# Kernel tuning notes

Hardware: AMD Instinct MI355X
Metric: run time of the kernel (lower is better)

## Reference

```python
import jax, jax.numpy as jnp
import numpy as np

T, N, DH, E = 4, 50000, 64, 800000
BN_EPS = 1e-5


def setup_inputs() -> dict:
    key = jax.random.key(0)
    ks = jax.random.split(key, 8)
    node_data = jax.random.normal(ks[0], (T, N, DH), dtype=jnp.float32)
    edge_weight = jax.random.uniform(ks[1], (E,), dtype=jnp.float32)
    W1 = jax.random.normal(ks[2], (DH, 3 * DH), dtype=jnp.float32) * 0.05
    b1 = jax.random.normal(ks[3], (DH,), dtype=jnp.float32) * 0.05
    gamma = jnp.ones((3 * DH,), dtype=jnp.float32)
    beta = jnp.zeros((3 * DH,), dtype=jnp.float32)
    src = jax.random.randint(ks[4], (E,), 0, N)
    dst = jax.random.randint(ks[5], (E,), 0, N)
    return {"node_data": node_data, "edge_weight": edge_weight, "W1": W1,
            "b1": b1, "gamma": gamma, "beta": beta, "src": src, "dst": dst}


def reference(node_data, edge_weight, W1, b1, gamma, beta, src, dst):
    # --- sparse weighted neighbor aggregation (torch.bmm with sparse ew) ---
    # msg[t, e, :] = w_e * x[t, src_e, :]
    msg = node_data[:, src, :] * edge_weight[None, :, None]          # [T, E, dh]
    agg = jnp.zeros((T, N, DH), jnp.float32).at[:, dst, :].add(msg)  # [T, N, dh]
    # Z = torch.sparse.sum(ew, dim=2); Z[Z==0]=1 (degree normalization)
    Z = jnp.zeros((N,), jnp.float32).at[dst].add(edge_weight)
    Z = jnp.where(Z == 0, 1.0, Z)
    avg_neighbor = agg / Z[None, :, None]
    # prev_state: zeros at t=0, shifted node_data otherwise
    prev = jnp.concatenate([jnp.zeros((1, N, DH), jnp.float32), node_data[:-1]], axis=0)
    inp = jnp.concatenate([node_data, prev, avg_neighbor], axis=2).reshape(T * N, 3 * DH)
    # --- ReluFCN with batchnorm (training-mode batch stats, biased var) ---
    mu = jnp.mean(inp, axis=0)
    var = jnp.mean(jnp.square(inp - mu), axis=0)
    xhat = (inp - mu) * jax.lax.rsqrt(var + BN_EPS) * gamma + beta
    out = jax.nn.relu(xhat @ W1.T + b1)
    return out.reshape(T, N, DH)
```

## Files before the change

kernel.cpp:

```cpp
#include <hip/hip_runtime.h>

#define TT 4
#define NN 50000
#define DH 64
#define EE 800000
#define BN_EPS 1e-5f
#define NB 196
#define G1 64
#define G2 256

typedef __attribute__((ext_vector_type(8))) short short8;
typedef __attribute__((ext_vector_type(4))) float floatx4;

#define WS_DEG      0
#define WS_FLAGS    200704
#define WS_ROWSTART 201728
#define WS_PX       401920
#define WS_PX2      467456
#define WS_PA       532992
#define WS_PA2      598528
#define WS_W1EFF    664064
#define WS_B1EFF    688640
#define WS_PACKED   1048576
#define WS_XB       8388608
#define WS_AVGB     34078720
#define WS_RANK     34078720

__device__ __forceinline__ unsigned short f2b(float f) {
    unsigned int u = __float_as_uint(f);
    unsigned int r = (u + 0x7FFFu + ((u >> 16) & 1u)) >> 16;
    return (unsigned short)r;
}
__device__ __forceinline__ float b2f(unsigned short u) {
    return __uint_as_float((unsigned int)u << 16);
}

__global__ __launch_bounds__(256) void k_prep_stats(
    const float* __restrict__ x, unsigned short* __restrict__ xb,
    float* __restrict__ PX, float* __restrict__ PX2,
    int* __restrict__ deg, int* __restrict__ flags) {
    int t = blockIdx.y;
    int tid = threadIdx.x;
    int pb = t * G1 + blockIdx.x;
    int gid = pb * 256 + tid;
    if (gid < NN) deg[gid] = 0;
    else if (gid < NN + NB) flags[gid - NN] = 0;

    int g = blockIdx.x * 256 + tid;
    const floatx4* xt = (const floatx4*)(x + (size_t)t * NN * 64);
    unsigned short* xbt = xb + (size_t)t * NN * 64;
    float s[4] = {0.f, 0.f, 0.f, 0.f}, s2[4] = {0.f, 0.f, 0.f, 0.f};
    for (int v = g; v < NN * 16; v += G1 * 256) {
        floatx4 d = __builtin_nontemporal_load(&xt[v]);
        ushort4 o;
        o.x = f2b(d.x); o.y = f2b(d.y); o.z = f2b(d.z); o.w = f2b(d.w);
        *(ushort4*)(xbt + (size_t)v * 4) = o;
        s[0] += d.x; s2[0] += d.x * d.x;
        s[1] += d.y; s2[1] += d.y * d.y;
        s[2] += d.z; s2[2] += d.z * d.z;
        s[3] += d.w; s2[3] += d.w * d.w;
    }
    __shared__ float ls[256 * 4], ls2[256 * 4];
#pragma unroll
    for (int j = 0; j < 4; ++j) { ls[tid * 4 + j] = s[j]; ls2[tid * 4 + j] = s2[j]; }
    __syncthreads();
    if (tid < 64) {
        int g16 = tid >> 2, comp = tid & 3;
        float rs = 0.f, rs2 = 0.f;
#pragma unroll
        for (int k = 0; k < 16; ++k) {
            int j = g16 + 16 * k;
            rs += ls[j * 4 + comp]; rs2 += ls2[j * 4 + comp];
        }
        int slot = (t * G1 + blockIdx.x) * 64 + tid;
        PX[slot] = rs; PX2[slot] = rs2;
    }
}

__global__ void k_rank(const int* __restrict__ dst, int* __restrict__ deg,
                       int* __restrict__ rank) {
    int e = blockIdx.x * 256 + threadIdx.x;
    if (e < EE) rank[e] = atomicAdd(&deg[dst[e]], 1);
}

__global__ __launch_bounds__(256) void k_scan_lb(
    const int* __restrict__ deg, int* __restrict__ flags,
    int* __restrict__ row_start) {
    int b = blockIdx.x, tid = threadIdx.x;
    int i = b * 256 + tid;
    int v = (i < NN) ? deg[i] : 0;
    __shared__ int ls[256];
    ls[tid] = v;
    __syncthreads();
    for (int off = 1; off < 256; off <<= 1) {
        int t = (tid >= off) ? ls[tid - off] : 0;
        __syncthreads();
        ls[tid] += t;
        __syncthreads();
    }
    int incl = ls[tid];
    if (tid == 0) atomicExch(&flags[b], ls[255] + 1);
    __shared__ int pre_s;
    if (tid == 0) pre_s = 0;
    __syncthreads();
    if (tid < b) {
        int f;
        do { f = atomicAdd(&flags[tid], 0); } while (f == 0);
        atomicAdd(&pre_s, f - 1);
    }
    __syncthreads();
    int excl = pre_s + incl - v;
    if (i < NN) row_start[i] = excl;
    if (i == NN - 1) row_start[NN] = excl + v;
}

__global__ void k_fill2(const int* __restrict__ src, const int* __restrict__ dst,
                        const float* __restrict__ ew, const int* __restrict__ rank,
                        const int* __restrict__ row_start, int2* __restrict__ packed) {
    int e = blockIdx.x * 256 + threadIdx.x;
    if (e < EE) {
        int p = row_start[dst[e]] + rank[e];
        packed[p] = make_int2(src[e], __float_as_int(ew[e]));
    }
}

__global__ __launch_bounds__(256) void k_agg(
    const unsigned short* __restrict__ xb, const int2* __restrict__ packed,
    const int* __restrict__ row_start, unsigned short* __restrict__ avgb) {
    int wv = __builtin_amdgcn_readfirstlane(threadIdx.x >> 6);
    int n = blockIdx.x * 4 + wv;
    int l = threadIdx.x & 63;
    int t = l >> 4;
    int cg = (l & 15) * 4;
    const unsigned short* xt = xb + (size_t)t * NN * 64 + cg;
    int rs = row_start[n], re = row_start[n + 1];
    float a0 = 0.f, a1 = 0.f, a2 = 0.f, a3 = 0.f, wsum = 0.f;
    int e = rs;
    for (; e + 8 <= re; e += 8) {
        int2 p[8];
        ushort4 v[8];
#pragma unroll
        for (int j = 0; j < 8; ++j) p[j] = packed[e + j];
#pragma unroll
        for (int j = 0; j < 8; ++j) v[j] = *(const ushort4*)(xt + (size_t)p[j].x * 64);
#pragma unroll
        for (int j = 0; j < 8; ++j) {
            float w = __int_as_float(p[j].y);
            wsum += w;
            a0 = fmaf(w, b2f(v[j].x), a0); a1 = fmaf(w, b2f(v[j].y), a1);
            a2 = fmaf(w, b2f(v[j].z), a2); a3 = fmaf(w, b2f(v[j].w), a3);
        }
    }
    for (; e < re; ++e) {
        int2 p0 = packed[e];
        float w0 = __int_as_float(p0.y);
        ushort4 v0 = *(const ushort4*)(xt + (size_t)p0.x * 64);
        wsum += w0;
        a0 = fmaf(w0, b2f(v0.x), a0); a1 = fmaf(w0, b2f(v0.y), a1);
        a2 = fmaf(w0, b2f(v0.z), a2); a3 = fmaf(w0, b2f(v0.w), a3);
    }
    float rz = (wsum == 0.f) ? 1.f : (1.f / wsum);
    ushort4 o;
    o.x = f2b(a0 * rz); o.y = f2b(a1 * rz); o.z = f2b(a2 * rz); o.w = f2b(a3 * rz);
    *(ushort4*)(avgb + (size_t)t * NN * 64 + (size_t)n * 64 + cg) = o;
}

__global__ __launch_bounds__(256) void k_stats_avg(
    const unsigned short* __restrict__ avgb, float* __restrict__ PA,
    float* __restrict__ PA2) {
    int tid = threadIdx.x;
    int g = blockIdx.x * 256 + tid;
    const short8* av = (const short8*)avgb;
    float s[8], s2[8];
#pragma unroll
    for (int j = 0; j < 8; ++j) { s[j] = 0.f; s2[j] = 0.f; }
    for (int v = g; v < TT * NN * 8; v += G2 * 256) {
        short8 d = av[v];
#pragma unroll
        for (int j = 0; j < 8; ++j) {
            float f = b2f((unsigned short)d[j]);
            s[j] += f; s2[j] += f * f;
        }
    }
    __shared__ float ls[256 * 8], ls2[256 * 8];
#pragma unroll
    for (int j = 0; j < 8; ++j) { ls[tid * 8 + j] = s[j]; ls2[tid * 8 + j] = s2[j]; }
    __syncthreads();
    if (tid < 64) {
        int g8 = tid >> 3, comp = tid & 7;
        float rs = 0.f, rs2 = 0.f;
#pragma unroll
        for (int k = 0; k < 32; ++k) {
            int j = g8 + 8 * k;
            rs += ls[j * 8 + comp]; rs2 += ls2[j * 8 + comp];
        }
        PA[blockIdx.x * 64 + tid] = rs;
        PA2[blockIdx.x * 64 + tid] = rs2;
    }
}

__global__ void k_fold(const float* __restrict__ W1, const float* __restrict__ b1,
                       const float* __restrict__ gamma, const float* __restrict__ beta,
                       const float* __restrict__ PX, const float* __restrict__ PX2,
                       const float* __restrict__ PA, const float* __restrict__ PA2,
                       unsigned short* __restrict__ W1eff, float* __restrict__ b1eff) {
    __shared__ float gS[192], hS[192];
    int c = threadIdx.x;
    const float inv = 1.0f / (float)(TT * NN);
    if (c < 192) {
        float s = 0.f, s2 = 0.f;
        if (c < 64) {
            for (int i = 0; i < TT * G1; ++i) { s += PX[i * 64 + c]; s2 += PX2[i * 64 + c]; }
        } else if (c < 128) {
            int cc = c - 64;
            for (int i = 0; i < (TT - 1) * G1; ++i) { s += PX[i * 64 + cc]; s2 += PX2[i * 64 + cc]; }
        } else {
            int cc = c - 128;
            for (int i = 0; i < G2; ++i) { s += PA[i * 64 + cc]; s2 += PA2[i * 64 + cc]; }
        }
        float mu = s * inv, ex2 = s2 * inv;
        float var = ex2 - mu * mu;
        float g = gamma[c] / sqrtf(var + BN_EPS);
        gS[c] = g;
        hS[c] = beta[c] - mu * g;
    }
    __syncthreads();
    for (int i = threadIdx.x; i < 64 * 192; i += blockDim.x) {
        int cc = i % 192;
        W1eff[i] = f2b(W1[i] * gS[cc]);
    }
    if (threadIdx.x < 64) {
        int o = threadIdx.x;
        float acc = b1[o];
        for (int cc = 0; cc < 192; ++cc) acc += hS[cc] * W1[o * 192 + cc];
        b1eff[o] = acc;
    }
}

__global__ __launch_bounds__(256) void k_main(
    const unsigned short* __restrict__ xb, const unsigned short* __restrict__ avgb,
    const unsigned short* __restrict__ Wb, const float* __restrict__ bias,
    float* __restrict__ out) {
    int wave = threadIdx.x >> 6;
    int lane = threadIdx.x & 63;
    int r0 = blockIdx.x * 64 + wave * 16;
    int m = lane & 15;
    int q = lane >> 4;

    const unsigned short* xrow = xb   + (size_t)(r0 + m) * 64 + q * 8;
    const unsigned short* prow = xb   + (size_t)(r0 - NN + m) * 64 + q * 8;
    const unsigned short* arow = avgb + (size_t)(r0 + m) * 64 + q * 8;
    bool has_prev = (r0 >= NN);

    floatx4 acc[4];
#pragma unroll
    for (int ct = 0; ct < 4; ++ct) acc[ct] = (floatx4){0.f, 0.f, 0.f, 0.f};

    const short8 zf = (short8){0, 0, 0, 0, 0, 0, 0, 0};

#pragma unroll
    for (int kc = 0; kc < 6; ++kc) {
        short8 a;
        if (kc < 2) {
            a = *(const short8*)(xrow + kc * 32);
        } else if (kc < 4) {
            a = has_prev ? *(const short8*)(prow + (kc - 2) * 32) : zf;
        } else {
            a = *(const short8*)(arow + (kc - 4) * 32);
        }
#pragma unroll
        for (int ct = 0; ct < 4; ++ct) {
            short8 b = *(const short8*)(Wb + (size_t)(ct * 16 + m) * 192 + kc * 32 + q * 8);
            acc[ct] = __builtin_amdgcn_mfma_f32_16x16x32_bf16(a, b, acc[ct], 0, 0, 0);
        }
    }

#pragma unroll
    for (int ct = 0; ct < 4; ++ct) {
        float bv = bias[ct * 16 + m];
#pragma unroll
        for (int i = 0; i < 4; ++i) {
            int row = q * 4 + i;
            __builtin_nontemporal_store(fmaxf(acc[ct][i] + bv, 0.f),
                                        &out[(size_t)(r0 + row) * 64 + ct * 16 + m]);
        }
    }
}

extern "C" void kernel_launch(void* const* d_in, const int* in_sizes, int n_in,
                              void* d_out, int out_size, void* d_ws, size_t ws_size,
                              hipStream_t stream) {
    const float* x     = (const float*)d_in[0];
    const float* ew    = (const float*)d_in[1];
    const float* W1    = (const float*)d_in[2];
    const float* b1    = (const float*)d_in[3];
    const float* gamma = (const float*)d_in[4];
    const float* beta  = (const float*)d_in[5];
    const int*   src   = (const int*)d_in[6];
    const int*   dst   = (const int*)d_in[7];
    float* out = (float*)d_out;
    char*  ws  = (char*)d_ws;

    int*   deg      = (int*)(ws + WS_DEG);
    int*   flags    = (int*)(ws + WS_FLAGS);
    int*   row_start= (int*)(ws + WS_ROWSTART);
    float* PX       = (float*)(ws + WS_PX);
    float* PX2      = (float*)(ws + WS_PX2);
    float* PA       = (float*)(ws + WS_PA);
    float* PA2      = (float*)(ws + WS_PA2);
    unsigned short* W1eff = (unsigned short*)(ws + WS_W1EFF);
    float* b1eff    = (float*)(ws + WS_B1EFF);
    int2*  packed   = (int2*)(ws + WS_PACKED);
    unsigned short* xb   = (unsigned short*)(ws + WS_XB);
    unsigned short* avgb = (unsigned short*)(ws + WS_AVGB);
    int*   rank     = (int*)(ws + WS_RANK);

    k_prep_stats<<<dim3(G1, TT), 256, 0, stream>>>(x, xb, PX, PX2, deg, flags);

    k_rank<<<(EE + 255) / 256, 256, 0, stream>>>(dst, deg, rank);

    k_scan_lb<<<NB, 256, 0, stream>>>(deg, flags, row_start);

    k_fill2<<<(EE + 255) / 256, 256, 0, stream>>>(src, dst, ew, rank, row_start, packed);

    k_agg<<<NN / 4, 256, 0, stream>>>(xb, packed, row_start, avgb);

    k_stats_avg<<<G2, 256, 0, stream>>>(avgb, PA, PA2);

    k_fold<<<1, 192, 0, stream>>>(W1, b1, gamma, beta, PX, PX2, PA, PA2, W1eff, b1eff);

    k_main<<<(TT * NN) / 64, 256, 0, stream>>>(xb, avgb, W1eff, b1eff, out);
}
```

Baseline: 338.3 us.

## Interleave timesteps per node in bf16 buffers so gathers fetch all T rows at once

The bf16 copy of node features and the averaged-neighbor buffer move from [T][N][64] to node-major [N][T][64], so each node's four timesteps sit in one contiguous 512-byte row. The aggregation kernel then gathers a whole row per edge with 16-byte loads, and has each half-wave take alternate edges before combining them with a cross-lane shuffle. This removes the four scattered 128-byte gathers per edge of the old layout. The matmul kernel's addressing is updated for the new layout, including the previous-timestep offset. The tail loop now issues a dummy load from row 0 for padded lanes, and the stats kernel over avgb still works because it only sums per-channel values.

```diff
diff --git a/kernel.cpp b/kernel.cpp
--- a/kernel.cpp
+++ b/kernel.cpp
@@ -48,13 +48,12 @@
 
     int g = blockIdx.x * 256 + tid;
     const floatx4* xt = (const floatx4*)(x + (size_t)t * NN * 64);
-    unsigned short* xbt = xb + (size_t)t * NN * 64;
     float s[4] = {0.f, 0.f, 0.f, 0.f}, s2[4] = {0.f, 0.f, 0.f, 0.f};
     for (int v = g; v < NN * 16; v += G1 * 256) {
         floatx4 d = __builtin_nontemporal_load(&xt[v]);
         ushort4 o;
         o.x = f2b(d.x); o.y = f2b(d.y); o.z = f2b(d.z); o.w = f2b(d.w);
-        *(ushort4*)(xbt + (size_t)v * 4) = o;
+        *(ushort4*)(xb + (size_t)(v >> 4) * 256 + t * 64 + (v & 15) * 4) = o;
         s[0] += d.x; s2[0] += d.x * d.x;
         s[1] += d.y; s2[1] += d.y * d.y;
         s[2] += d.z; s2[2] += d.z * d.z;
@@ -127,42 +126,72 @@
 __global__ __launch_bounds__(256) void k_agg(
     const unsigned short* __restrict__ xb, const int2* __restrict__ packed,
     const int* __restrict__ row_start, unsigned short* __restrict__ avgb) {
-    int wv = __builtin_amdgcn_readfirstlane(threadIdx.x >> 6);
+    int wv = threadIdx.x >> 6;
     int n = blockIdx.x * 4 + wv;
     int l = threadIdx.x & 63;
-    int t = l >> 4;
-    int cg = (l & 15) * 4;
-    const unsigned short* xt = xb + (size_t)t * NN * 64 + cg;
+    int half = l >> 5;
+    int j = l & 31;
+    const unsigned short* xt = xb + (size_t)j * 8;
     int rs = row_start[n], re = row_start[n + 1];
-    float a0 = 0.f, a1 = 0.f, a2 = 0.f, a3 = 0.f, wsum = 0.f;
-    int e = rs;
-    for (; e + 8 <= re; e += 8) {
-        int2 p[8];
-        ushort4 v[8];
-#pragma unroll
-        for (int j = 0; j < 8; ++j) p[j] = packed[e + j];
-#pragma unroll
-        for (int j = 0; j < 8; ++j) v[j] = *(const ushort4*)(xt + (size_t)p[j].x * 64);
-#pragma unroll
-        for (int j = 0; j < 8; ++j) {
-            float w = __int_as_float(p[j].y);
+    float acc[8];
+#pragma unroll
+    for (int k = 0; k < 8; ++k) acc[k] = 0.f;
+    float wsum = 0.f;
+
+    int base = rs;
+    for (; base + 16 <= re; base += 16) {
+        int2 p[8]; short8 v[8];
+#pragma unroll
+        for (int i = 0; i < 8; ++i) p[i] = packed[base + 2 * i + half];
+#pragma unroll
+        for (int i = 0; i < 8; ++i) v[i] = *(const short8*)(xt + (size_t)p[i].x * 256);
+#pragma unroll
+        for (int i = 0; i < 8; ++i) {
+            float w = __int_as_float(p[i].y);
             wsum += w;
-            a0 = fmaf(w, b2f(v[j].x), a0); a1 = fmaf(w, b2f(v[j].y), a1);
-            a2 = fmaf(w, b2f(v[j].z), a2); a3 = fmaf(w, b2f(v[j].w), a3);
-        }
-    }
-    for (; e < re; ++e) {
-        int2 p0 = packed[e];
-        float w0 = __int_as_float(p0.y);
-        ushort4 v0 = *(const ushort4*)(xt + (size_t)p0.x * 64);
-        wsum += w0;
-        a0 = fmaf(w0, b2f(v0.x), a0); a1 = fmaf(w0, b2f(v0.y), a1);
-        a2 = fmaf(w0, b2f(v0.z), a2); a3 = fmaf(w0, b2f(v0.w), a3);
-    }
+#pragma unroll
+            for (int k = 0; k < 8; ++k)
+                acc[k] = fmaf(w, b2f((unsigned short)v[i][k]), acc[k]);
+        }
+    }
+    if (base + 8 <= re) {
+        int2 p[4]; short8 v[4];
+#pragma unroll
+        for (int i = 0; i < 4; ++i) p[i] = packed[base + 2 * i + half];
+#pragma unroll
+        for (int i = 0; i < 4; ++i) v[i] = *(const short8*)(xt + (size_t)p[i].x * 256);
+#pragma unroll
+        for (int i = 0; i < 4; ++i) {
+            float w = __int_as_float(p[i].y);
+            wsum += w;
+#pragma unroll
+            for (int k = 0; k < 8; ++k)
+                acc[k] = fmaf(w, b2f((unsigned short)v[i][k]), acc[k]);
+        }
+        base += 8;
+    }
+    for (; base < re; base += 2) {
+        int ee = base + half;
+        int2 p = (ee < re) ? packed[ee] : make_int2(0, 0);
+        short8 v = *(const short8*)(xt + (size_t)p.x * 256);
+        float w = __int_as_float(p.y);
+        wsum += w;
+#pragma unroll
+        for (int k = 0; k < 8; ++k)
+            acc[k] = fmaf(w, b2f((unsigned short)v[k]), acc[k]);
+    }
+
+#pragma unroll
+    for (int k = 0; k < 8; ++k) acc[k] += __shfl_xor(acc[k], 32);
+    wsum += __shfl_xor(wsum, 32);
+
     float rz = (wsum == 0.f) ? 1.f : (1.f / wsum);
-    ushort4 o;
-    o.x = f2b(a0 * rz); o.y = f2b(a1 * rz); o.z = f2b(a2 * rz); o.w = f2b(a3 * rz);
-    *(ushort4*)(avgb + (size_t)t * NN * 64 + (size_t)n * 64 + cg) = o;
+    if (half == 0) {
+        short8 o;
+#pragma unroll
+        for (int k = 0; k < 8; ++k) o[k] = (short)f2b(acc[k] * rz);
+        *(short8*)(avgb + (size_t)n * 256 + (size_t)j * 8) = o;
+    }
 }
 
 __global__ __launch_bounds__(256) void k_stats_avg(
@@ -244,13 +273,15 @@
     int wave = threadIdx.x >> 6;
     int lane = threadIdx.x & 63;
     int r0 = blockIdx.x * 64 + wave * 16;
+    int t = r0 / NN;
+    int n0 = r0 - t * NN;
     int m = lane & 15;
     int q = lane >> 4;
 
-    const unsigned short* xrow = xb   + (size_t)(r0 + m) * 64 + q * 8;
-    const unsigned short* prow = xb   + (size_t)(r0 - NN + m) * 64 + q * 8;
-    const unsigned short* arow = avgb + (size_t)(r0 + m) * 64 + q * 8;
-    bool has_prev = (r0 >= NN);
+    size_t nb = (size_t)(n0 + m) * 256 + (size_t)t * 64 + q * 8;
+    const unsigned short* xrow = xb + nb;
+    const unsigned short* arow = avgb + nb;
+    bool has_prev = (t >= 1);
 
     floatx4 acc[4];
 #pragma unroll
@@ -264,7 +295,7 @@
         if (kc < 2) {
             a = *(const short8*)(xrow + kc * 32);
         } else if (kc < 4) {
-            a = has_prev ? *(const short8*)(prow + (kc - 2) * 32) : zf;
+            a = has_prev ? *(const short8*)(xrow - 64 + (kc - 2) * 32) : zf;
         } else {
             a = *(const short8*)(arow + (kc - 4) * 32);
         }
```

After: 342.9 us. Within noise of the previous version (+1.4%).

## Interleave timesteps per node in bf16 buffers and switch kernels to grid-stride loops

Applied to the files above, without the earlier changes.

The bf16 copies of node features and neighbour averages move from a [T][N][64] layout to a node-major [N][T][64] layout. Each edge gather in the aggregation kernel then reads one contiguous 512-byte row covering all timesteps, instead of four separate 128-byte rows. The rank, fill, aggregation and matmul kernels become persistent grid-stride loops over a fixed number of blocks, and the aggregation inner loop masks its tail instead of using a separate remainder loop. The weight-folding kernel is spread over several blocks, each of which recomputes the batchnorm statistics.

```diff
diff --git a/kernel.cpp b/kernel.cpp
--- a/kernel.cpp
+++ b/kernel.cpp
@@ -8,6 +8,11 @@
 #define NB 196
 #define G1 64
 #define G2 256
+#define EB 2048
+#define AGG_B 2048
+#define AGG_W (AGG_B*4)
+#define MAIN_B 2048
+#define FOLD_B 8
 
 typedef __attribute__((ext_vector_type(8))) short short8;
 typedef __attribute__((ext_vector_type(4))) float floatx4;
@@ -48,13 +53,12 @@
 
     int g = blockIdx.x * 256 + tid;
     const floatx4* xt = (const floatx4*)(x + (size_t)t * NN * 64);
-    unsigned short* xbt = xb + (size_t)t * NN * 64;
     float s[4] = {0.f, 0.f, 0.f, 0.f}, s2[4] = {0.f, 0.f, 0.f, 0.f};
     for (int v = g; v < NN * 16; v += G1 * 256) {
         floatx4 d = __builtin_nontemporal_load(&xt[v]);
         ushort4 o;
         o.x = f2b(d.x); o.y = f2b(d.y); o.z = f2b(d.z); o.w = f2b(d.w);
-        *(ushort4*)(xbt + (size_t)v * 4) = o;
+        *(ushort4*)(xb + (size_t)(v >> 4) * 256 + t * 64 + (v & 15) * 4) = o;
         s[0] += d.x; s2[0] += d.x * d.x;
         s[1] += d.y; s2[1] += d.y * d.y;
         s[2] += d.z; s2[2] += d.z * d.z;
@@ -77,10 +81,11 @@
     }
 }
 
-__global__ void k_rank(const int* __restrict__ dst, int* __restrict__ deg,
-                       int* __restrict__ rank) {
-    int e = blockIdx.x * 256 + threadIdx.x;
-    if (e < EE) rank[e] = atomicAdd(&deg[dst[e]], 1);
+__global__ __launch_bounds__(256) void k_rank(const int* __restrict__ dst,
+                                              int* __restrict__ deg,
+                                              int* __restrict__ rank) {
+    for (int e = blockIdx.x * 256 + threadIdx.x; e < EE; e += EB * 256)
+        rank[e] = atomicAdd(&deg[dst[e]], 1);
 }
 
 __global__ __launch_bounds__(256) void k_scan_lb(
@@ -114,11 +119,11 @@
     if (i == NN - 1) row_start[NN] = excl + v;
 }
 
-__global__ void k_fill2(const int* __restrict__ src, const int* __restrict__ dst,
-                        const float* __restrict__ ew, const int* __restrict__ rank,
-                        const int* __restrict__ row_start, int2* __restrict__ packed) {
-    int e = blockIdx.x * 256 + threadIdx.x;
-    if (e < EE) {
+__global__ __launch_bounds__(256) void k_fill2(
+    const int* __restrict__ src, const int* __restrict__ dst,
+    const float* __restrict__ ew, const int* __restrict__ rank,
+    const int* __restrict__ row_start, int2* __restrict__ packed) {
+    for (int e = blockIdx.x * 256 + threadIdx.x; e < EE; e += EB * 256) {
         int p = row_start[dst[e]] + rank[e];
         packed[p] = make_int2(src[e], __float_as_int(ew[e]));
     }
@@ -128,41 +133,39 @@
     const unsigned short* __restrict__ xb, const int2* __restrict__ packed,
     const int* __restrict__ row_start, unsigned short* __restrict__ avgb) {
     int wv = __builtin_amdgcn_readfirstlane(threadIdx.x >> 6);
-    int n = blockIdx.x * 4 + wv;
     int l = threadIdx.x & 63;
-    int t = l >> 4;
-    int cg = (l & 15) * 4;
-    const unsigned short* xt = xb + (size_t)t * NN * 64 + cg;
-    int rs = row_start[n], re = row_start[n + 1];
-    float a0 = 0.f, a1 = 0.f, a2 = 0.f, a3 = 0.f, wsum = 0.f;
-    int e = rs;
-    for (; e + 8 <= re; e += 8) {
-        int2 p[8];
-        ushort4 v[8];
-#pragma unroll
-        for (int j = 0; j < 8; ++j) p[j] = packed[e + j];
-#pragma unroll
-        for (int j = 0; j < 8; ++j) v[j] = *(const ushort4*)(xt + (size_t)p[j].x * 64);
-#pragma unroll
-        for (int j = 0; j < 8; ++j) {
-            float w = __int_as_float(p[j].y);
-            wsum += w;
-            a0 = fmaf(w, b2f(v[j].x), a0); a1 = fmaf(w, b2f(v[j].y), a1);
-            a2 = fmaf(w, b2f(v[j].z), a2); a3 = fmaf(w, b2f(v[j].w), a3);
-        }
-    }
-    for (; e < re; ++e) {
-        int2 p0 = packed[e];
-        float w0 = __int_as_float(p0.y);
-        ushort4 v0 = *(const ushort4*)(xt + (size_t)p0.x * 64);
-        wsum += w0;
-        a0 = fmaf(w0, b2f(v0.x), a0); a1 = fmaf(w0, b2f(v0.y), a1);
-        a2 = fmaf(w0, b2f(v0.z), a2); a3 = fmaf(w0, b2f(v0.w), a3);
-    }
-    float rz = (wsum == 0.f) ? 1.f : (1.f / wsum);
-    ushort4 o;
-    o.x = f2b(a0 * rz); o.y = f2b(a1 * rz); o.z = f2b(a2 * rz); o.w = f2b(a3 * rz);
-    *(ushort4*)(avgb + (size_t)t * NN * 64 + (size_t)n * 64 + cg) = o;
+    int wgid = blockIdx.x * 4 + wv;
+    const ushort4* xl = (const ushort4*)xb + l;
+    for (int n = wgid; n < NN; n += AGG_W) {
+        int rs = row_start[n], re = row_start[n + 1];
+        float a0 = 0.f, a1 = 0.f, a2 = 0.f, a3 = 0.f, wsum = 0.f;
+        for (int e = rs; e < re; e += 8) {
+            int rem = re - e;
+            int2 p[8];
+#pragma unroll
+            for (int j = 0; j < 8; ++j) p[j] = packed[e + j];
+            ushort4 v[8];
+#pragma unroll
+            for (int j = 0; j < 8; ++j) {
+                int sidx = (j < rem) ? p[j].x : 0;
+                v[j] = xl[(size_t)sidx * 64];
+            }
+#pragma unroll
+            for (int j = 0; j < 8; ++j) {
+                float w = (j < rem) ? __int_as_float(p[j].y) : 0.f;
+                wsum += w;
+                a0 = fmaf(w, b2f(v[j].x), a0);
+                a1 = fmaf(w, b2f(v[j].y), a1);
+                a2 = fmaf(w, b2f(v[j].z), a2);
+                a3 = fmaf(w, b2f(v[j].w), a3);
+            }
+        }
+        float rz = (wsum == 0.f) ? 1.f : (1.f / wsum);
+        ushort4 o;
+        o.x = f2b(a0 * rz); o.y = f2b(a1 * rz);
+        o.z = f2b(a2 * rz); o.w = f2b(a3 * rz);
+        *((ushort4*)avgb + (size_t)n * 64 + l) = o;
+    }
 }
 
 __global__ __launch_bounds__(256) void k_stats_avg(
@@ -225,12 +228,10 @@
         hS[c] = beta[c] - mu * g;
     }
     __syncthreads();
-    for (int i = threadIdx.x; i < 64 * 192; i += blockDim.x) {
-        int cc = i % 192;
-        W1eff[i] = f2b(W1[i] * gS[cc]);
-    }
-    if (threadIdx.x < 64) {
-        int o = threadIdx.x;
+    for (int i = blockIdx.x * 192 + c; i < 64 * 192; i += FOLD_B * 192)
+        W1eff[i] = f2b(W1[i] * gS[c]);
+    if (c < 8) {
+        int o = blockIdx.x * 8 + c;
         float acc = b1[o];
         for (int cc = 0; cc < 192; ++cc) acc += hS[cc] * W1[o * 192 + cc];
         b1eff[o] = acc;
@@ -243,46 +244,50 @@
     float* __restrict__ out) {
     int wave = threadIdx.x >> 6;
     int lane = threadIdx.x & 63;
-    int r0 = blockIdx.x * 64 + wave * 16;
     int m = lane & 15;
     int q = lane >> 4;
-
-    const unsigned short* xrow = xb   + (size_t)(r0 + m) * 64 + q * 8;
-    const unsigned short* prow = xb   + (size_t)(r0 - NN + m) * 64 + q * 8;
-    const unsigned short* arow = avgb + (size_t)(r0 + m) * 64 + q * 8;
-    bool has_prev = (r0 >= NN);
-
-    floatx4 acc[4];
-#pragma unroll
-    for (int ct = 0; ct < 4; ++ct) acc[ct] = (floatx4){0.f, 0.f, 0.f, 0.f};
-
     const short8 zf = (short8){0, 0, 0, 0, 0, 0, 0, 0};
 
-#pragma unroll
-    for (int kc = 0; kc < 6; ++kc) {
-        short8 a;
-        if (kc < 2) {
-            a = *(const short8*)(xrow + kc * 32);
-        } else if (kc < 4) {
-            a = has_prev ? *(const short8*)(prow + (kc - 2) * 32) : zf;
-        } else {
-            a = *(const short8*)(arow + (kc - 4) * 32);
-        }
+    for (int tile = blockIdx.x; tile < (TT * NN) / 64; tile += MAIN_B) {
+        int r0 = tile * 64 + wave * 16;
+        int t = r0 / NN;
+        int n0 = r0 - t * NN;
+
+        size_t nb = (size_t)(n0 + m) * 256 + (size_t)t * 64 + q * 8;
+        const unsigned short* xrow = xb + nb;
+        const unsigned short* arow = avgb + nb;
+        bool has_prev = (t >= 1);
+
+        floatx4 acc[4];
+#pragma unroll
+        for (int ct = 0; ct < 4; ++ct) acc[ct] = (floatx4){0.f, 0.f, 0.f, 0.f};
+
+#pragma unroll
+        for (int kc = 0; kc < 6; ++kc) {
+            short8 a;
+            if (kc < 2) {
+                a = *(const short8*)(xrow + kc * 32);
+            } else if (kc < 4) {
+                a = has_prev ? *(const short8*)(xrow - 64 + (kc - 2) * 32) : zf;
+            } else {
+                a = *(const short8*)(arow + (kc - 4) * 32);
+            }
+#pragma unroll
+            for (int ct = 0; ct < 4; ++ct) {
+                short8 b = *(const short8*)(Wb + (size_t)(ct * 16 + m) * 192 + kc * 32 + q * 8);
+                acc[ct] = __builtin_amdgcn_mfma_f32_16x16x32_bf16(a, b, acc[ct], 0, 0, 0);
+            }
+        }
+
 #pragma unroll
         for (int ct = 0; ct < 4; ++ct) {
-            short8 b = *(const short8*)(Wb + (size_t)(ct * 16 + m) * 192 + kc * 32 + q * 8);
-            acc[ct] = __builtin_amdgcn_mfma_f32_16x16x32_bf16(a, b, acc[ct], 0, 0, 0);
-        }
-    }
-
-#pragma unroll
-    for (int ct = 0; ct < 4; ++ct) {
-        float bv = bias[ct * 16 + m];
-#pragma unroll
-        for (int i = 0; i < 4; ++i) {
-            int row = q * 4 + i;
-            __builtin_nontemporal_store(fmaxf(acc[ct][i] + bv, 0.f),
-                                        &out[(size_t)(r0 + row) * 64 + ct * 16 + m]);
+            float bv = bias[ct * 16 + m];
+#pragma unroll
+            for (int i = 0; i < 4; ++i) {
+                int row = q * 4 + i;
+                __builtin_nontemporal_store(fmaxf(acc[ct][i] + bv, 0.f),
+                                            &out[(size_t)(r0 + row) * 64 + ct * 16 + m]);
+            }
         }
     }
 }
@@ -317,17 +322,17 @@
 
     k_prep_stats<<<dim3(G1, TT), 256, 0, stream>>>(x, xb, PX, PX2, deg, flags);
 
-    k_rank<<<(EE + 255) / 256, 256, 0, stream>>>(dst, deg, rank);
+    k_rank<<<EB, 256, 0, stream>>>(dst, deg, rank);
 
     k_scan_lb<<<NB, 256, 0, stream>>>(deg, flags, row_start);
 
-    k_fill2<<<(EE + 255) / 256, 256, 0, stream>>>(src, dst, ew, rank, row_start, packed);
-
-    k_agg<<<NN / 4, 256, 0, stream>>>(xb, packed, row_start, avgb);
+    k_fill2<<<EB, 256, 0, stream>>>(src, dst, ew, rank, row_start, packed);
+
+    k_agg<<<AGG_B, 256, 0, stream>>>(xb, packed, row_start, avgb);
 
     k_stats_avg<<<G2, 256, 0, stream>>>(avgb, PA, PA2);
 
-    k_fold<<<1, 192, 0, stream>>>(W1, b1, gamma, beta, PX, PX2, PA, PA2, W1eff, b1eff);
-
-    k_main<<<(TT * NN) / 64, 256, 0, stream>>>(xb, avgb, W1eff, b1eff, out);
-}
+    k_fold<<<FOLD_B, 192, 0, stream>>>(W1, b1, gamma, beta, PX, PX2, PA, PA2, W1eff, b1eff);
+
+    k_main<<<MAIN_B, 256, 0, stream>>>(xb, avgb, W1eff, b1eff, out);
+}
```

Measured after the change: 316.1 us. 1.07x faster.
